# Optimization experiments

Measured on AMD Instinct MI355X. Metric: run time of the kernel, lower is better.

## Reference

```python
import jax, jax.numpy as jnp
import numpy as np

B, N, IN_C, HID_C, OUT_C = 8, 2048, 128, 256, 32


def setup_inputs() -> dict:
    key = jax.random.key(0)
    ks = jax.random.split(key, 8)
    s1 = 1.0 / np.sqrt(IN_C)
    s2 = 1.0 / np.sqrt(HID_C)
    return {
        "x": jax.random.normal(ks[0], (B, N, IN_C), dtype=jnp.float32),
        "A": jax.random.randint(ks[1], (B, N, N), 0, 2, dtype=jnp.int32),
        "W1_l": jax.random.normal(ks[2], (IN_C, HID_C), dtype=jnp.float32) * s1,
        "W1_r": jax.random.normal(ks[3], (IN_C, HID_C), dtype=jnp.float32) * s1,
        "b1": jnp.zeros((HID_C,), dtype=jnp.float32),
        "W2_l": jax.random.normal(ks[4], (HID_C, OUT_C), dtype=jnp.float32) * s2,
        "W2_r": jax.random.normal(ks[5], (HID_C, OUT_C), dtype=jnp.float32) * s2,
        "b2": jnp.zeros((OUT_C,), dtype=jnp.float32),
    }


def _mean_agg(mask, deg_inv, h):
    # edge (i, j) means source i -> target j (PyG source_to_target flow):
    # agg[b, j] = mean over i with A[b, i, j] != 0 of h[b, i]
    return jnp.einsum("bij,bid->bjd", mask, h) * deg_inv


def reference(x, A, W1_l, W1_r, b1, W2_l, W2_r, b2):
    mask = (A != 0).astype(x.dtype)            # [B, N, N]
    deg = jnp.sum(mask, axis=1)                # in-degree per target node, [B, N]
    deg_inv = (1.0 / jnp.maximum(deg, 1.0))[..., None]  # isolated nodes -> 0 agg

    # SAGEConv 1: lin_l(mean_agg(x)) + lin_r(x) + bias, then ReLU
    # (dropout p=0.2 is inactive in eval mode)
    h = _mean_agg(mask, deg_inv, x) @ W1_l + x @ W1_r + b1
    h = jax.nn.relu(h)

    # SAGEConv 2
    out = _mean_agg(mask, deg_inv, h) @ W2_l + h @ W2_r + b2  # [B, N, OUT_C]
    return (jax.nn.log_softmax(out, axis=-1), out)
```

## Files before the change

kernel.cpp:

```cpp
#include <hip/hip_runtime.h>


#define B_   8
#define N_   2048
#define INC  128
#define HID  256
#define OUTC 32

typedef __attribute__((ext_vector_type(8))) __bf16 bf16x8;
typedef __attribute__((ext_vector_type(4))) float f32x4;
typedef __attribute__((ext_vector_type(4))) unsigned int u32x4;
typedef __attribute__((ext_vector_type(2))) unsigned int u32x2;

__device__ __forceinline__ unsigned short f2bf(float f) {
  unsigned int u = __float_as_uint(f);
  u += 0x7FFFu + ((u >> 16) & 1u);
  return (unsigned short)(u >> 16);
}

__device__ __forceinline__ f32x4 mfma16(bf16x8 a, bf16x8 b, f32x4 c) {
  return __builtin_amdgcn_mfma_f32_16x16x32_bf16(a, b, c, 0, 0, 0);
}

__device__ __forceinline__ bf16x8 ones_frag() {
  union { unsigned short u[8]; bf16x8 v; } o;
#pragma unroll
  for (int i = 0; i < 8; i++) o.u[i] = 0x3F80;
  return o.v;
}

__device__ __forceinline__ void lut_init(u32x2* lut, int t) {
  if (t < 16) {
    unsigned int w0 = (t & 1 ? 0x3F80u : 0u) | (t & 2 ? 0x3F800000u : 0u);
    unsigned int w1 = (t & 4 ? 0x3F80u : 0u) | (t & 8 ? 0x3F800000u : 0u);
    u32x2 e = {w0, w1};
    lut[t] = e;
  }
}

__global__ __launch_bounds__(256, 8) void k_bits(
    const int* __restrict__ A, unsigned int* __restrict__ bits) {
  const int t = threadIdx.x;
  const int w = t >> 6, l = t & 63;
  const int gw = blockIdx.x * 4 + w;
  const int b = gw >> 10;
  const int it = (gw >> 5) & 31, jt = gw & 31;
  const int i0 = it * 64, j0 = jt * 64;
  const int* Ap = A + ((size_t)(b * N_) + i0) * N_ + j0 + l;
  unsigned long long col = 0;
#pragma unroll 8
  for (int r = 0; r < 64; r++) {
    int a = Ap[(size_t)r * N_];
    unsigned long long m = __ballot(a != 0);
    col |= ((m >> l) & 1ull) << r;
  }
  *reinterpret_cast<unsigned long long*>(
      bits + ((size_t)(b * N_) + j0 + l) * 64 + (i0 >> 5)) = col;
}

__global__ __launch_bounds__(256) void k_prep_small(
    const float* __restrict__ x,
    const float* __restrict__ W1l, const float* __restrict__ W1r,
    const float* __restrict__ W2l, const float* __restrict__ W2r,
    unsigned short* __restrict__ xT, unsigned short* __restrict__ acat1,
    unsigned short* __restrict__ W1cT, unsigned short* __restrict__ W2cT) {
  const int bx = blockIdx.x, t = threadIdx.x;
  if (bx < 256) {
    __shared__ unsigned short xls[128 * 72];
    const int b = bx >> 5, it = bx & 31, i0 = it * 64;
    const int dq = (t & 31) * 4;
    const int irow = t >> 5;
#pragma unroll
    for (int s = 0; s < 8; s++) {
      int il = s * 8 + irow;
      int i = i0 + il;
      f32x4 v = *reinterpret_cast<const f32x4*>(x + ((size_t)(b * N_ + i)) * INC + dq);
      unsigned int p0 = f2bf(v[0]) | ((unsigned int)f2bf(v[1]) << 16);
      unsigned int p1 = f2bf(v[2]) | ((unsigned int)f2bf(v[3]) << 16);
      u32x2 pk = {p0, p1};
      *reinterpret_cast<u32x2*>(acat1 + ((size_t)(b * N_ + i)) * HID + 128 + dq) = pk;
      xls[(dq + 0) * 72 + il] = f2bf(v[0]);
      xls[(dq + 1) * 72 + il] = f2bf(v[1]);
      xls[(dq + 2) * 72 + il] = f2bf(v[2]);
      xls[(dq + 3) * 72 + il] = f2bf(v[3]);
    }
    __syncthreads();
    const int d = t >> 1, half = t & 1;
    const u32x4* src = reinterpret_cast<const u32x4*>(&xls[d * 72 + half * 32]);
    u32x4* dst = reinterpret_cast<u32x4*>(xT + ((size_t)(b * INC + d)) * N_ + i0 + half * 32);
#pragma unroll
    for (int q = 0; q < 4; q++) dst[q] = src[q];
  } else if (bx < 320) {
    int base = (bx - 256) * 1024 + t * 4;
#pragma unroll
    for (int q = 0; q < 4; q++) {
      int id = base + q;
      int e = id >> 8, k = id & 255;
      float v = (k < 128) ? W1l[k * 256 + e] : W1r[(k - 128) * 256 + e];
      W1cT[id] = f2bf(v);
    }
  } else {
    int base = (bx - 320) * 1024 + t * 4;
#pragma unroll
    for (int q = 0; q < 4; q++) {
      int id = base + q;
      int n = id >> 8, k = id & 255;
      float v = (n < 32) ? W2l[k * 32 + n] : W2r[k * 32 + (n - 32)];
      W2cT[id] = f2bf(v);
    }
  }
}

__global__ __launch_bounds__(256, 4) void k_agg1(
    const unsigned int* __restrict__ bits, const unsigned short* __restrict__ xT,
    unsigned short* __restrict__ acat1, float* __restrict__ deg_inv) {
  __shared__ u32x2 lut[16];
  __shared__ __align__(16) float part[4][8][64][4];
  __shared__ __align__(16) float pdeg[4][16][4];
  const int t = threadIdx.x;
  const int w = t >> 6, l = t & 63, lr = l & 15, lq = l >> 4;
  lut_init(lut, t);
  __syncthreads();
  const int b = blockIdx.y, j0 = blockIdx.x * 16;
  const unsigned int* bp = bits + ((size_t)(b * N_ + j0 + lr)) * 64 + w * 16;
  const unsigned short* xb = xT + (size_t)b * INC * N_ + w * 512;

  const f32x4 zero = {0.f, 0.f, 0.f, 0.f};
  f32x4 acc[8] = {zero, zero, zero, zero, zero, zero, zero, zero};
  f32x4 dacc = zero;
  const bf16x8 onesf = ones_frag();

  for (int s = 0; s < 16; s++) {
    unsigned int w32 = bp[s];
    unsigned int bval = (w32 >> (lq * 8)) & 0xFFu;
    union { u32x2 u2[2]; bf16x8 v; } af;
    af.u2[0] = lut[bval & 15u];
    af.u2[1] = lut[bval >> 4];
    dacc = mfma16(af.v, onesf, dacc);
#pragma unroll
    for (int ds = 0; ds < 8; ds++) {
      bf16x8 bfr = *reinterpret_cast<const bf16x8*>(
          xb + ((size_t)(ds * 16 + lr)) * N_ + s * 32 + lq * 8);
      acc[ds] = mfma16(af.v, bfr, acc[ds]);
    }
  }

#pragma unroll
  for (int ds = 0; ds < 8; ds++)
    *reinterpret_cast<f32x4*>(&part[w][ds][l][0]) = acc[ds];
  if (lr == 0) *reinterpret_cast<f32x4*>(&pdeg[w][lq][0]) = dacc;
  __syncthreads();

  float dinv[4];
#pragma unroll
  for (int r = 0; r < 4; r++) {
    float deg = pdeg[0][lq][r] + pdeg[1][lq][r] + pdeg[2][lq][r] + pdeg[3][lq][r];
    dinv[r] = 1.0f / fmaxf(deg, 1.0f);
  }
  if (w == 0 && lr == 0) {
#pragma unroll
    for (int r = 0; r < 4; r++)
      deg_inv[b * N_ + j0 + lq * 4 + r] = dinv[r];
  }
  unsigned short* ag = acat1 + ((size_t)(b * N_ + j0)) * HID;
#pragma unroll
  for (int dd = 0; dd < 2; dd++) {
    int ds = w * 2 + dd;
    f32x4 v0 = *reinterpret_cast<f32x4*>(&part[0][ds][l][0]);
    f32x4 v1 = *reinterpret_cast<f32x4*>(&part[1][ds][l][0]);
    f32x4 v2 = *reinterpret_cast<f32x4*>(&part[2][ds][l][0]);
    f32x4 v3 = *reinterpret_cast<f32x4*>(&part[3][ds][l][0]);
#pragma unroll
    for (int r = 0; r < 4; r++)
      ag[(size_t)(lq * 4 + r) * HID + ds * 16 + lr] =
          f2bf((v0[r] + v1[r] + v2[r] + v3[r]) * dinv[r]);
  }
}

__global__ __launch_bounds__(256, 4) void k_dense2(
    const unsigned short* __restrict__ acat1, const unsigned short* __restrict__ W1cT,
    const unsigned short* __restrict__ W2cT, const float* __restrict__ b1,
    const float* __restrict__ b2, unsigned short* __restrict__ hlT,
    float* __restrict__ hr) {
  __shared__ __align__(16) unsigned short hs[16 * 264];
  const int t = threadIdx.x;
  const int w = t >> 6, l = t & 63, lr = l & 15, lq = l >> 4;
  const int b = blockIdx.y, j0 = blockIdx.x * 16;
  const unsigned short* ab = acat1 + ((size_t)(b * N_ + j0 + lr)) * HID;
  const int e0 = w * 64;

  const f32x4 zero = {0.f, 0.f, 0.f, 0.f};
  f32x4 acc[4] = {zero, zero, zero, zero};
#pragma unroll
  for (int ks = 0; ks < 8; ks++) {
    bf16x8 af = *reinterpret_cast<const bf16x8*>(ab + ks * 32 + lq * 8);
#pragma unroll
    for (int es = 0; es < 4; es++) {
      bf16x8 bfr = *reinterpret_cast<const bf16x8*>(
          W1cT + ((size_t)(e0 + es * 16 + lr)) * HID + ks * 32 + lq * 8);
      acc[es] = mfma16(af, bfr, acc[es]);
    }
  }
#pragma unroll
  for (int es = 0; es < 4; es++) {
    int e = e0 + es * 16 + lr;
    float bias = b1[e];
#pragma unroll
    for (int r = 0; r < 4; r++)
      hs[(lq * 4 + r) * 264 + e] = f2bf(fmaxf(acc[es][r] + bias, 0.0f));
  }
  __syncthreads();

  f32x4 a2 = zero;
#pragma unroll
  for (int ks = 0; ks < 8; ks++) {
    bf16x8 af = *reinterpret_cast<const bf16x8*>(&hs[lr * 264 + ks * 32 + lq * 8]);
    bf16x8 bfr = *reinterpret_cast<const bf16x8*>(
        W2cT + ((size_t)(w * 16 + lr)) * HID + ks * 32 + lq * 8);
    a2 = mfma16(af, bfr, a2);
  }
  if (w < 2) {
    int c = w * 16 + lr;
    unsigned int p0 = f2bf(a2[0]) | ((unsigned int)f2bf(a2[1]) << 16);
    unsigned int p1 = f2bf(a2[2]) | ((unsigned int)f2bf(a2[3]) << 16);
    u32x2 pk = {p0, p1};
    *reinterpret_cast<u32x2*>(hlT + ((size_t)(b * 32 + c)) * N_ + j0 + lq * 4) = pk;
  } else {
    int c = (w - 2) * 16 + lr;
    float bias = b2[c];
#pragma unroll
    for (int r = 0; r < 4; r++)
      hr[((size_t)(b * N_ + j0 + lq * 4 + r)) * OUTC + c] = a2[r] + bias;
  }
}

__global__ __launch_bounds__(256, 4) void k_agg2out(
    const unsigned int* __restrict__ bits, const unsigned short* __restrict__ hlT,
    const float* __restrict__ deg_inv, const float* __restrict__ hr,
    float* __restrict__ out) {
  __shared__ u32x2 lut[16];
  __shared__ __align__(16) float part[4][64][2][4];
  const int t = threadIdx.x;
  const int w = t >> 6, l = t & 63, lr = l & 15, lq = l >> 4;
  lut_init(lut, t);
  __syncthreads();
  const int b = blockIdx.y, j0 = blockIdx.x * 16;
  const unsigned int* bp = bits + ((size_t)(b * N_ + j0 + lr)) * 64 + w * 16;
  const unsigned short* hb = hlT + (size_t)b * 32 * N_ + w * 512;

  const f32x4 zero = {0.f, 0.f, 0.f, 0.f};
  f32x4 acc[2] = {zero, zero};

  for (int s = 0; s < 16; s++) {
    unsigned int w32 = bp[s];
    unsigned int bval = (w32 >> (lq * 8)) & 0xFFu;
    union { u32x2 u2[2]; bf16x8 v; } af;
    af.u2[0] = lut[bval & 15u];
    af.u2[1] = lut[bval >> 4];
#pragma unroll
    for (int cs = 0; cs < 2; cs++) {
      bf16x8 bfr = *reinterpret_cast<const bf16x8*>(
          hb + ((size_t)(cs * 16 + lr)) * N_ + s * 32 + lq * 8);
      acc[cs] = mfma16(af.v, bfr, acc[cs]);
    }
  }

  *reinterpret_cast<f32x4*>(&part[w][l][0][0]) = acc[0];
  *reinterpret_cast<f32x4*>(&part[w][l][1][0]) = acc[1];
  __syncthreads();

  if (w == 0) {
    const size_t SZ = (size_t)B_ * N_ * OUTC;
#pragma unroll
    for (int r = 0; r < 4; r++) {
      int j = j0 + lq * 4 + r;
      float dv = deg_inv[b * N_ + j];
      size_t base = ((size_t)(b * N_ + j)) * OUTC;
      float v0 = (part[0][l][0][r] + part[1][l][0][r] +
                  part[2][l][0][r] + part[3][l][0][r]) * dv + hr[base + lr];
      float v1 = (part[0][l][1][r] + part[1][l][1][r] +
                  part[2][l][1][r] + part[3][l][1][r]) * dv + hr[base + 16 + lr];
      float m = fmaxf(v0, v1);
#pragma unroll
      for (int d = 1; d < 16; d <<= 1) m = fmaxf(m, __shfl_xor(m, d, 64));
      float s = __expf(v0 - m) + __expf(v1 - m);
#pragma unroll
      for (int d = 1; d < 16; d <<= 1) s += __shfl_xor(s, d, 64);
      float ls = m + __logf(s);
      out[base + lr] = v0 - ls;
      out[base + 16 + lr] = v1 - ls;
      out[SZ + base + lr] = v0;
      out[SZ + base + 16 + lr] = v1;
    }
  }
}

extern "C" void kernel_launch(void* const* d_in, const int* in_sizes, int n_in,
                              void* d_out, int out_size, void* d_ws, size_t ws_size,
                              hipStream_t stream) {
  (void)in_sizes; (void)n_in; (void)out_size; (void)ws_size;
  const float* x   = (const float*)d_in[0];
  const int*   A   = (const int*)d_in[1];
  const float* W1l = (const float*)d_in[2];
  const float* W1r = (const float*)d_in[3];
  const float* b1  = (const float*)d_in[4];
  const float* W2l = (const float*)d_in[5];
  const float* W2r = (const float*)d_in[6];
  const float* b2  = (const float*)d_in[7];
  float* out = (float*)d_out;

  char* ws = (char*)d_ws;
  unsigned short* W1cT    = (unsigned short*)(ws + 0);
  unsigned short* W2cT    = (unsigned short*)(ws + 131072);
  float*          deg_inv = (float*)(ws + 163840);
  unsigned int*   bits    = (unsigned int*)(ws + 229376);
  unsigned short* xT      = (unsigned short*)(ws + 4423680);
  unsigned short* hlT     = (unsigned short*)(ws + 4423680);
  float*          hr      = (float*)(ws + 5472256);
  unsigned short* acat1   = (unsigned short*)(ws + 8617984);

  k_bits      <<<dim3(2048),   dim3(256), 0, stream>>>(A, bits);
  k_prep_small<<<dim3(336),    dim3(256), 0, stream>>>(x, W1l, W1r, W2l, W2r,
                                                       xT, acat1, W1cT, W2cT);
  k_agg1      <<<dim3(128, 8), dim3(256), 0, stream>>>(bits, xT, acat1, deg_inv);
  k_dense2    <<<dim3(128, 8), dim3(256), 0, stream>>>(acat1, W1cT, W2cT, b1, b2,
                                                       hlT, hr);
  k_agg2out   <<<dim3(128, 8), dim3(256), 0, stream>>>(bits, hlT, deg_inv, hr, out);
}
```

Measured before the change: 321.7 us.

## Merge bitmask and prep kernels; process 32 target nodes per block

Folds the adjacency-bitmask kernel and the small prep kernel into one launch using block-index ranges, removing one kernel launch. The aggregation and dense kernels now handle two 16-row tiles of target nodes per block, so each loaded x/h fragment feeds two MFMAs and the reduction of partial sums through shared memory is reshaped (wave 0 keeps its own partials in registers). This halves the grid to 512 blocks and raises register use per thread, lowering occupancy in exchange for more reuse. The merged prep kernel also allocates the transpose shared buffer in every block, which can limit occupancy of the bitmask part.

```diff
diff --git a/kernel.cpp b/kernel.cpp
--- a/kernel.cpp
+++ b/kernel.cpp
@@ -38,36 +38,41 @@
   }
 }
 
-__global__ __launch_bounds__(256, 8) void k_bits(
-    const int* __restrict__ A, unsigned int* __restrict__ bits) {
-  const int t = threadIdx.x;
-  const int w = t >> 6, l = t & 63;
-  const int gw = blockIdx.x * 4 + w;
-  const int b = gw >> 10;
-  const int it = (gw >> 5) & 31, jt = gw & 31;
-  const int i0 = it * 64, j0 = jt * 64;
-  const int* Ap = A + ((size_t)(b * N_) + i0) * N_ + j0 + l;
-  unsigned long long col = 0;
-#pragma unroll 8
-  for (int r = 0; r < 64; r++) {
-    int a = Ap[(size_t)r * N_];
-    unsigned long long m = __ballot(a != 0);
-    col |= ((m >> l) & 1ull) << r;
-  }
-  *reinterpret_cast<unsigned long long*>(
-      bits + ((size_t)(b * N_) + j0 + l) * 64 + (i0 >> 5)) = col;
-}
-
-__global__ __launch_bounds__(256) void k_prep_small(
-    const float* __restrict__ x,
+__device__ __forceinline__ bf16x8 expand8(const u32x2* lut, unsigned int bval) {
+  union { u32x2 u2[2]; bf16x8 v; } af;
+  af.u2[0] = lut[bval & 15u];
+  af.u2[1] = lut[bval >> 4];
+  return af.v;
+}
+
+__global__ __launch_bounds__(256, 8) void k_prep(
+    const int* __restrict__ A, const float* __restrict__ x,
     const float* __restrict__ W1l, const float* __restrict__ W1r,
     const float* __restrict__ W2l, const float* __restrict__ W2r,
-    unsigned short* __restrict__ xT, unsigned short* __restrict__ acat1,
+    unsigned int* __restrict__ bits, unsigned short* __restrict__ xT,
+    unsigned short* __restrict__ acat1,
     unsigned short* __restrict__ W1cT, unsigned short* __restrict__ W2cT) {
+  __shared__ unsigned short xls[128 * 72];
   const int bx = blockIdx.x, t = threadIdx.x;
-  if (bx < 256) {
-    __shared__ unsigned short xls[128 * 72];
-    const int b = bx >> 5, it = bx & 31, i0 = it * 64;
+  if (bx < 2048) {
+    const int w = t >> 6, l = t & 63;
+    const int gw = bx * 4 + w;
+    const int b = gw >> 10;
+    const int it = (gw >> 5) & 31, jt = gw & 31;
+    const int i0 = it * 64, j0 = jt * 64;
+    const int* Ap = A + ((size_t)(b * N_) + i0) * N_ + j0 + l;
+    unsigned long long col = 0;
+#pragma unroll 8
+    for (int r = 0; r < 64; r++) {
+      int a = Ap[(size_t)r * N_];
+      unsigned long long m = __ballot(a != 0);
+      col |= ((m >> l) & 1ull) << r;
+    }
+    *reinterpret_cast<unsigned long long*>(
+        bits + ((size_t)(b * N_) + j0 + l) * 64 + (i0 >> 5)) = col;
+  } else if (bx < 2304) {
+    const int bb = bx - 2048;
+    const int b = bb >> 5, it = bb & 31, i0 = it * 64;
     const int dq = (t & 31) * 4;
     const int irow = t >> 5;
 #pragma unroll
@@ -90,8 +95,8 @@
     u32x4* dst = reinterpret_cast<u32x4*>(xT + ((size_t)(b * INC + d)) * N_ + i0 + half * 32);
 #pragma unroll
     for (int q = 0; q < 4; q++) dst[q] = src[q];
-  } else if (bx < 320) {
-    int base = (bx - 256) * 1024 + t * 4;
+  } else if (bx < 2368) {
+    int base = (bx - 2304) * 1024 + t * 4;
 #pragma unroll
     for (int q = 0; q < 4; q++) {
       int id = base + q;
@@ -100,7 +105,7 @@
       W1cT[id] = f2bf(v);
     }
   } else {
-    int base = (bx - 320) * 1024 + t * 4;
+    int base = (bx - 2368) * 1024 + t * 4;
 #pragma unroll
     for (int q = 0; q < 4; q++) {
       int id = base + q;
@@ -111,187 +116,221 @@
   }
 }
 
-__global__ __launch_bounds__(256, 4) void k_agg1(
+__global__ __launch_bounds__(256, 2) void k_agg1(
     const unsigned int* __restrict__ bits, const unsigned short* __restrict__ xT,
     unsigned short* __restrict__ acat1, float* __restrict__ deg_inv) {
   __shared__ u32x2 lut[16];
-  __shared__ __align__(16) float part[4][8][64][4];
-  __shared__ __align__(16) float pdeg[4][16][4];
+  __shared__ __align__(16) float part[3][2][8][64][4];
+  __shared__ __align__(16) float pdeg[3][2][16][4];
   const int t = threadIdx.x;
   const int w = t >> 6, l = t & 63, lr = l & 15, lq = l >> 4;
   lut_init(lut, t);
   __syncthreads();
-  const int b = blockIdx.y, j0 = blockIdx.x * 16;
-  const unsigned int* bp = bits + ((size_t)(b * N_ + j0 + lr)) * 64 + w * 16;
+  const int b = blockIdx.y, j0 = blockIdx.x * 32;
+  const unsigned int* bp0 = bits + ((size_t)(b * N_ + j0 + lr)) * 64 + w * 16;
+  const unsigned int* bp1 = bp0 + (size_t)16 * 64;
   const unsigned short* xb = xT + (size_t)b * INC * N_ + w * 512;
 
   const f32x4 zero = {0.f, 0.f, 0.f, 0.f};
-  f32x4 acc[8] = {zero, zero, zero, zero, zero, zero, zero, zero};
-  f32x4 dacc = zero;
+  f32x4 acc[2][8];
+#pragma unroll
+  for (int jt = 0; jt < 2; jt++)
+#pragma unroll
+    for (int ds = 0; ds < 8; ds++) acc[jt][ds] = zero;
+  f32x4 dacc[2] = {zero, zero};
   const bf16x8 onesf = ones_frag();
 
   for (int s = 0; s < 16; s++) {
-    unsigned int w32 = bp[s];
-    unsigned int bval = (w32 >> (lq * 8)) & 0xFFu;
-    union { u32x2 u2[2]; bf16x8 v; } af;
-    af.u2[0] = lut[bval & 15u];
-    af.u2[1] = lut[bval >> 4];
-    dacc = mfma16(af.v, onesf, dacc);
+    bf16x8 af0 = expand8(lut, (bp0[s] >> (lq * 8)) & 0xFFu);
+    bf16x8 af1 = expand8(lut, (bp1[s] >> (lq * 8)) & 0xFFu);
+    dacc[0] = mfma16(af0, onesf, dacc[0]);
+    dacc[1] = mfma16(af1, onesf, dacc[1]);
 #pragma unroll
     for (int ds = 0; ds < 8; ds++) {
       bf16x8 bfr = *reinterpret_cast<const bf16x8*>(
           xb + ((size_t)(ds * 16 + lr)) * N_ + s * 32 + lq * 8);
-      acc[ds] = mfma16(af.v, bfr, acc[ds]);
-    }
-  }
-
-#pragma unroll
-  for (int ds = 0; ds < 8; ds++)
-    *reinterpret_cast<f32x4*>(&part[w][ds][l][0]) = acc[ds];
-  if (lr == 0) *reinterpret_cast<f32x4*>(&pdeg[w][lq][0]) = dacc;
-  __syncthreads();
-
-  float dinv[4];
-#pragma unroll
-  for (int r = 0; r < 4; r++) {
-    float deg = pdeg[0][lq][r] + pdeg[1][lq][r] + pdeg[2][lq][r] + pdeg[3][lq][r];
-    dinv[r] = 1.0f / fmaxf(deg, 1.0f);
-  }
-  if (w == 0 && lr == 0) {
-#pragma unroll
-    for (int r = 0; r < 4; r++)
-      deg_inv[b * N_ + j0 + lq * 4 + r] = dinv[r];
-  }
+      acc[0][ds] = mfma16(af0, bfr, acc[0][ds]);
+      acc[1][ds] = mfma16(af1, bfr, acc[1][ds]);
+    }
+  }
+
+  if (w > 0) {
+#pragma unroll
+    for (int jt = 0; jt < 2; jt++) {
+#pragma unroll
+      for (int ds = 0; ds < 8; ds++)
+        *reinterpret_cast<f32x4*>(&part[w - 1][jt][ds][l][0]) = acc[jt][ds];
+      if (lr == 0) *reinterpret_cast<f32x4*>(&pdeg[w - 1][jt][lq][0]) = dacc[jt];
+    }
+  }
+  __syncthreads();
+  if (w != 0) return;
+
   unsigned short* ag = acat1 + ((size_t)(b * N_ + j0)) * HID;
 #pragma unroll
-  for (int dd = 0; dd < 2; dd++) {
-    int ds = w * 2 + dd;
-    f32x4 v0 = *reinterpret_cast<f32x4*>(&part[0][ds][l][0]);
-    f32x4 v1 = *reinterpret_cast<f32x4*>(&part[1][ds][l][0]);
-    f32x4 v2 = *reinterpret_cast<f32x4*>(&part[2][ds][l][0]);
-    f32x4 v3 = *reinterpret_cast<f32x4*>(&part[3][ds][l][0]);
-#pragma unroll
-    for (int r = 0; r < 4; r++)
-      ag[(size_t)(lq * 4 + r) * HID + ds * 16 + lr] =
-          f2bf((v0[r] + v1[r] + v2[r] + v3[r]) * dinv[r]);
-  }
-}
-
-__global__ __launch_bounds__(256, 4) void k_dense2(
+  for (int jt = 0; jt < 2; jt++) {
+    float dinv[4];
+#pragma unroll
+    for (int r = 0; r < 4; r++) {
+      float deg = dacc[jt][r] + pdeg[0][jt][lq][r] + pdeg[1][jt][lq][r] +
+                  pdeg[2][jt][lq][r];
+      dinv[r] = 1.0f / fmaxf(deg, 1.0f);
+    }
+    if (lr == 0) {
+#pragma unroll
+      for (int r = 0; r < 4; r++)
+        deg_inv[b * N_ + j0 + jt * 16 + lq * 4 + r] = dinv[r];
+    }
+#pragma unroll
+    for (int ds = 0; ds < 8; ds++) {
+      f32x4 v0 = *reinterpret_cast<f32x4*>(&part[0][jt][ds][l][0]);
+      f32x4 v1 = *reinterpret_cast<f32x4*>(&part[1][jt][ds][l][0]);
+      f32x4 v2 = *reinterpret_cast<f32x4*>(&part[2][jt][ds][l][0]);
+#pragma unroll
+      for (int r = 0; r < 4; r++)
+        ag[(size_t)(jt * 16 + lq * 4 + r) * HID + ds * 16 + lr] =
+            f2bf((acc[jt][ds][r] + v0[r] + v1[r] + v2[r]) * dinv[r]);
+    }
+  }
+}
+
+__global__ __launch_bounds__(256, 2) void k_dense2(
     const unsigned short* __restrict__ acat1, const unsigned short* __restrict__ W1cT,
     const unsigned short* __restrict__ W2cT, const float* __restrict__ b1,
     const float* __restrict__ b2, unsigned short* __restrict__ hlT,
     float* __restrict__ hr) {
-  __shared__ __align__(16) unsigned short hs[16 * 264];
+  __shared__ __align__(16) unsigned short hs[32 * 264];
   const int t = threadIdx.x;
   const int w = t >> 6, l = t & 63, lr = l & 15, lq = l >> 4;
-  const int b = blockIdx.y, j0 = blockIdx.x * 16;
-  const unsigned short* ab = acat1 + ((size_t)(b * N_ + j0 + lr)) * HID;
+  const int b = blockIdx.y, j0 = blockIdx.x * 32;
   const int e0 = w * 64;
 
   const f32x4 zero = {0.f, 0.f, 0.f, 0.f};
-  f32x4 acc[4] = {zero, zero, zero, zero};
+  f32x4 acc[2][4];
+#pragma unroll
+  for (int jt = 0; jt < 2; jt++)
+#pragma unroll
+    for (int es = 0; es < 4; es++) acc[jt][es] = zero;
+
 #pragma unroll
   for (int ks = 0; ks < 8; ks++) {
-    bf16x8 af = *reinterpret_cast<const bf16x8*>(ab + ks * 32 + lq * 8);
+    bf16x8 af0 = *reinterpret_cast<const bf16x8*>(
+        acat1 + ((size_t)(b * N_ + j0 + lr)) * HID + ks * 32 + lq * 8);
+    bf16x8 af1 = *reinterpret_cast<const bf16x8*>(
+        acat1 + ((size_t)(b * N_ + j0 + 16 + lr)) * HID + ks * 32 + lq * 8);
 #pragma unroll
     for (int es = 0; es < 4; es++) {
       bf16x8 bfr = *reinterpret_cast<const bf16x8*>(
           W1cT + ((size_t)(e0 + es * 16 + lr)) * HID + ks * 32 + lq * 8);
-      acc[es] = mfma16(af, bfr, acc[es]);
-    }
-  }
-#pragma unroll
-  for (int es = 0; es < 4; es++) {
-    int e = e0 + es * 16 + lr;
-    float bias = b1[e];
-#pragma unroll
-    for (int r = 0; r < 4; r++)
-      hs[(lq * 4 + r) * 264 + e] = f2bf(fmaxf(acc[es][r] + bias, 0.0f));
-  }
-  __syncthreads();
-
-  f32x4 a2 = zero;
+      acc[0][es] = mfma16(af0, bfr, acc[0][es]);
+      acc[1][es] = mfma16(af1, bfr, acc[1][es]);
+    }
+  }
+#pragma unroll
+  for (int jt = 0; jt < 2; jt++)
+#pragma unroll
+    for (int es = 0; es < 4; es++) {
+      int e = e0 + es * 16 + lr;
+      float bias = b1[e];
+#pragma unroll
+      for (int r = 0; r < 4; r++)
+        hs[(jt * 16 + lq * 4 + r) * 264 + e] = f2bf(fmaxf(acc[jt][es][r] + bias, 0.0f));
+    }
+  __syncthreads();
+
+  const int jt = w & 1, nh = w >> 1;
+  f32x4 a2[2] = {zero, zero};
 #pragma unroll
   for (int ks = 0; ks < 8; ks++) {
-    bf16x8 af = *reinterpret_cast<const bf16x8*>(&hs[lr * 264 + ks * 32 + lq * 8]);
-    bf16x8 bfr = *reinterpret_cast<const bf16x8*>(
-        W2cT + ((size_t)(w * 16 + lr)) * HID + ks * 32 + lq * 8);
-    a2 = mfma16(af, bfr, a2);
-  }
-  if (w < 2) {
-    int c = w * 16 + lr;
-    unsigned int p0 = f2bf(a2[0]) | ((unsigned int)f2bf(a2[1]) << 16);
-    unsigned int p1 = f2bf(a2[2]) | ((unsigned int)f2bf(a2[3]) << 16);
-    u32x2 pk = {p0, p1};
-    *reinterpret_cast<u32x2*>(hlT + ((size_t)(b * 32 + c)) * N_ + j0 + lq * 4) = pk;
+    bf16x8 af = *reinterpret_cast<const bf16x8*>(&hs[(jt * 16 + lr) * 264 + ks * 32 + lq * 8]);
+#pragma unroll
+    for (int ns = 0; ns < 2; ns++) {
+      bf16x8 bfr = *reinterpret_cast<const bf16x8*>(
+          W2cT + ((size_t)(nh * 32 + ns * 16 + lr)) * HID + ks * 32 + lq * 8);
+      a2[ns] = mfma16(af, bfr, a2[ns]);
+    }
+  }
+  if (nh == 0) {
+#pragma unroll
+    for (int ns = 0; ns < 2; ns++) {
+      int c = ns * 16 + lr;
+      unsigned int p0 = f2bf(a2[ns][0]) | ((unsigned int)f2bf(a2[ns][1]) << 16);
+      unsigned int p1 = f2bf(a2[ns][2]) | ((unsigned int)f2bf(a2[ns][3]) << 16);
+      u32x2 pk = {p0, p1};
+      *reinterpret_cast<u32x2*>(
+          hlT + ((size_t)(b * 32 + c)) * N_ + j0 + jt * 16 + lq * 4) = pk;
+    }
   } else {
-    int c = (w - 2) * 16 + lr;
-    float bias = b2[c];
-#pragma unroll
-    for (int r = 0; r < 4; r++)
-      hr[((size_t)(b * N_ + j0 + lq * 4 + r)) * OUTC + c] = a2[r] + bias;
-  }
-}
-
-__global__ __launch_bounds__(256, 4) void k_agg2out(
+#pragma unroll
+    for (int ns = 0; ns < 2; ns++) {
+      int c = ns * 16 + lr;
+      float bias = b2[c];
+#pragma unroll
+      for (int r = 0; r < 4; r++)
+        hr[((size_t)(b * N_ + j0 + jt * 16 + lq * 4 + r)) * OUTC + c] = a2[ns][r] + bias;
+    }
+  }
+}
+
+__global__ __launch_bounds__(256, 2) void k_agg2out(
     const unsigned int* __restrict__ bits, const unsigned short* __restrict__ hlT,
     const float* __restrict__ deg_inv, const float* __restrict__ hr,
     float* __restrict__ out) {
   __shared__ u32x2 lut[16];
-  __shared__ __align__(16) float part[4][64][2][4];
+  __shared__ __align__(16) float part[4][2][2][64][4];
   const int t = threadIdx.x;
   const int w = t >> 6, l = t & 63, lr = l & 15, lq = l >> 4;
   lut_init(lut, t);
   __syncthreads();
-  const int b = blockIdx.y, j0 = blockIdx.x * 16;
-  const unsigned int* bp = bits + ((size_t)(b * N_ + j0 + lr)) * 64 + w * 16;
+  const int b = blockIdx.y, j0 = blockIdx.x * 32;
+  const unsigned int* bp0 = bits + ((size_t)(b * N_ + j0 + lr)) * 64 + w * 16;
+  const unsigned int* bp1 = bp0 + (size_t)16 * 64;
   const unsigned short* hb = hlT + (size_t)b * 32 * N_ + w * 512;
 
   const f32x4 zero = {0.f, 0.f, 0.f, 0.f};
-  f32x4 acc[2] = {zero, zero};
+  f32x4 acc[2][2] = {{zero, zero}, {zero, zero}};
 
   for (int s = 0; s < 16; s++) {
-    unsigned int w32 = bp[s];
-    unsigned int bval = (w32 >> (lq * 8)) & 0xFFu;
-    union { u32x2 u2[2]; bf16x8 v; } af;
-    af.u2[0] = lut[bval & 15u];
-    af.u2[1] = lut[bval >> 4];
+    bf16x8 af0 = expand8(lut, (bp0[s] >> (lq * 8)) & 0xFFu);
+    bf16x8 af1 = expand8(lut, (bp1[s] >> (lq * 8)) & 0xFFu);
 #pragma unroll
     for (int cs = 0; cs < 2; cs++) {
       bf16x8 bfr = *reinterpret_cast<const bf16x8*>(
           hb + ((size_t)(cs * 16 + lr)) * N_ + s * 32 + lq * 8);
-      acc[cs] = mfma16(af.v, bfr, acc[cs]);
-    }
-  }
-
-  *reinterpret_cast<f32x4*>(&part[w][l][0][0]) = acc[0];
-  *reinterpret_cast<f32x4*>(&part[w][l][1][0]) = acc[1];
-  __syncthreads();
-
-  if (w == 0) {
-    const size_t SZ = (size_t)B_ * N_ * OUTC;
-#pragma unroll
-    for (int r = 0; r < 4; r++) {
-      int j = j0 + lq * 4 + r;
-      float dv = deg_inv[b * N_ + j];
-      size_t base = ((size_t)(b * N_ + j)) * OUTC;
-      float v0 = (part[0][l][0][r] + part[1][l][0][r] +
-                  part[2][l][0][r] + part[3][l][0][r]) * dv + hr[base + lr];
-      float v1 = (part[0][l][1][r] + part[1][l][1][r] +
-                  part[2][l][1][r] + part[3][l][1][r]) * dv + hr[base + 16 + lr];
-      float m = fmaxf(v0, v1);
-#pragma unroll
-      for (int d = 1; d < 16; d <<= 1) m = fmaxf(m, __shfl_xor(m, d, 64));
-      float s = __expf(v0 - m) + __expf(v1 - m);
-#pragma unroll
-      for (int d = 1; d < 16; d <<= 1) s += __shfl_xor(s, d, 64);
-      float ls = m + __logf(s);
-      out[base + lr] = v0 - ls;
-      out[base + 16 + lr] = v1 - ls;
-      out[SZ + base + lr] = v0;
-      out[SZ + base + 16 + lr] = v1;
-    }
+      acc[0][cs] = mfma16(af0, bfr, acc[0][cs]);
+      acc[1][cs] = mfma16(af1, bfr, acc[1][cs]);
+    }
+  }
+#pragma unroll
+  for (int jt = 0; jt < 2; jt++)
+#pragma unroll
+    for (int cs = 0; cs < 2; cs++)
+      *reinterpret_cast<f32x4*>(&part[w][jt][cs][l][0]) = acc[jt][cs];
+  __syncthreads();
+  if (w >= 2) return;
+
+  const int jt = w;
+  const size_t SZ = (size_t)B_ * N_ * OUTC;
+#pragma unroll
+  for (int r = 0; r < 4; r++) {
+    int j = j0 + jt * 16 + lq * 4 + r;
+    float dv = deg_inv[b * N_ + j];
+    size_t base = ((size_t)(b * N_ + j)) * OUTC;
+    float v0 = (part[0][jt][0][l][r] + part[1][jt][0][l][r] +
+                part[2][jt][0][l][r] + part[3][jt][0][l][r]) * dv + hr[base + lr];
+    float v1 = (part[0][jt][1][l][r] + part[1][jt][1][l][r] +
+                part[2][jt][1][l][r] + part[3][jt][1][l][r]) * dv + hr[base + 16 + lr];
+    float m = fmaxf(v0, v1);
+#pragma unroll
+    for (int d = 1; d < 16; d <<= 1) m = fmaxf(m, __shfl_xor(m, d, 64));
+    float s = __expf(v0 - m) + __expf(v1 - m);
+#pragma unroll
+    for (int d = 1; d < 16; d <<= 1) s += __shfl_xor(s, d, 64);
+    float ls = m + __logf(s);
+    out[base + lr] = v0 - ls;
+    out[base + 16 + lr] = v1 - ls;
+    out[SZ + base + lr] = v0;
+    out[SZ + base + 16 + lr] = v1;
   }
 }
 
@@ -319,11 +358,10 @@
   float*          hr      = (float*)(ws + 5472256);
   unsigned short* acat1   = (unsigned short*)(ws + 8617984);
 
-  k_bits      <<<dim3(2048),   dim3(256), 0, stream>>>(A, bits);
-  k_prep_small<<<dim3(336),    dim3(256), 0, stream>>>(x, W1l, W1r, W2l, W2r,
-                                                       xT, acat1, W1cT, W2cT);
-  k_agg1      <<<dim3(128, 8), dim3(256), 0, stream>>>(bits, xT, acat1, deg_inv);
-  k_dense2    <<<dim3(128, 8), dim3(256), 0, stream>>>(acat1, W1cT, W2cT, b1, b2,
-                                                       hlT, hr);
-  k_agg2out   <<<dim3(128, 8), dim3(256), 0, stream>>>(bits, hlT, deg_inv, hr, out);
-}
+  k_prep   <<<dim3(2384),  dim3(256), 0, stream>>>(A, x, W1l, W1r, W2l, W2r,
+                                                   bits, xT, acat1, W1cT, W2cT);
+  k_agg1   <<<dim3(64, 8), dim3(256), 0, stream>>>(bits, xT, acat1, deg_inv);
+  k_dense2 <<<dim3(64, 8), dim3(256), 0, stream>>>(acat1, W1cT, W2cT, b1, b2,
+                                                   hlT, hr);
+  k_agg2out<<<dim3(64, 8), dim3(256), 0, stream>>>(bits, hlT, deg_inv, hr, out);
+}
```

Result: faster. 287.8 us (-10.5%).
